# Kernel optimization log

Measured on AMD Instinct MI355X. Metric: run time of the kernel, lower is better.

Reference implementation:

```python
import jax, jax.numpy as jnp
import numpy as np

S, B, P, E = 2048, 128, 1024, 192  # seq len, batch, single_eval_pos, embedding_size
NAN_IND, INF_IND, NEG_INF_IND = -2.0, 2.0, 4.0


def setup_inputs() -> dict:
    key = jax.random.key(0)
    k1, k2, k3 = jax.random.split(key, 3)
    y = jax.random.normal(k1, (S, B, 1), jnp.float32)
    # nn.Linear(in_features=2, out_features=E): weight [E, 2], bias [E]
    W = jax.random.normal(k2, (E, 2), jnp.float32) * 0.1
    b = jax.random.normal(k3, (E,), jnp.float32) * 0.1
    return {"y": y, "W": W, "b": b, "single_eval_pos": P}


def reference(y, W, b, single_eval_pos):
    sep = single_eval_pos
    # --- nan handling (nan_handling_y_encoder=True) ---
    prefix = y[:sep]                              # [P, B, 1]
    means = jnp.nanmean(prefix, axis=0)           # [B, 1] (torch.nanmean ignores NaN only)
    is_nan = jnp.isnan(y)
    is_inf = jnp.isinf(y)
    mask = is_nan | is_inf
    indicators = (is_nan * NAN_IND
                  + (is_inf & (y > 0)) * INF_IND
                  + (is_inf & (y < 0)) * NEG_INF_IND).astype(y.dtype)  # [S, B, 1]
    y_imp = jnp.where(mask, means[None], y)       # [S, B, 1]

    # --- multiclass rank encode (max_num_classes >= 2) ---
    # torch: rank[t,b] = #{distinct values v in train prefix of column b : v < y[t,b]}
    col = y_imp[..., 0]                           # [S, B]
    s = jnp.sort(col[:sep], axis=0)               # [P, B] sorted train prefix per batch
    # marker of first occurrence of each distinct value in the sorted prefix
    is_new = jnp.concatenate(
        [jnp.ones((1, s.shape[1]), bool), s[1:] != s[:-1]], axis=0)  # [P, B]
    # [S, P, B] boolean compare, masked to distinct values, reduce over P
    cmp = (col[:, None, :] > s[None, :, :]) & is_new[None]
    ranks = cmp.sum(axis=1).astype(y.dtype)[..., None]  # [S, B, 1]

    x = jnp.concatenate([ranks, indicators], axis=-1)   # [S, B, 2]
    return x @ W.T + b                                   # [S, B, E]
```

## Files before the change

### kernel.cpp

```cpp
#include <hip/hip_runtime.h>
#include <math.h>

#define S_DIM 2048
#define B_DIM 128
#define P_DIM 1024
#define E_DIM 192
#define SB    (S_DIM * B_DIM)

typedef float f32x4 __attribute__((ext_vector_type(4)));
typedef float f32x2 __attribute__((ext_vector_type(2)));

__global__ __launch_bounds__(256) void prep_rank_kernel(
    const float* __restrict__ y, const int* __restrict__ sep_p,
    f32x2* __restrict__ ri) {
  __shared__ float sm[P_DIM];
  __shared__ float su[P_DIM];
  __shared__ float redf[256];
  __shared__ int   redi[256];
  __shared__ int   scan[256];
  __shared__ int   Ksh;

  const int b   = blockIdx.x;
  const int tid = threadIdx.x;
  const int sep = *sep_p;

  float lsum = 0.f;
  int   lcnt = 0;
  for (int i = tid; i < P_DIM; i += 256) {
    float v = (i < sep) ? y[i * B_DIM + b] : INFINITY;
    sm[i] = v;
    if (i < sep && !isnan(v)) { lsum += v; lcnt++; }
  }
  redf[tid] = lsum;
  redi[tid] = lcnt;
  __syncthreads();
  for (int off = 128; off > 0; off >>= 1) {
    if (tid < off) { redf[tid] += redf[tid + off]; redi[tid] += redi[tid + off]; }
    __syncthreads();
  }
  const float mean = redf[0] / (float)redi[0];

  for (int i = tid; i < sep; i += 256) {
    float v = sm[i];
    if (isnan(v) || isinf(v)) sm[i] = mean;
  }
  __syncthreads();

  for (int k = 2; k <= P_DIM; k <<= 1) {
    for (int j = k >> 1; j > 0; j >>= 1) {
      for (int i = tid; i < P_DIM; i += 256) {
        int ixj = i ^ j;
        if (ixj > i) {
          float a = sm[i], c = sm[ixj];
          bool up = ((i & k) == 0);
          if (up ? (a > c) : (a < c)) { sm[i] = c; sm[ixj] = a; }
        }
      }
      __syncthreads();
    }
  }

  int flags[4];
  int lu = 0;
  for (int q = 0; q < 4; q++) {
    int i = tid * 4 + q;
    bool nw = (i == 0) || (sm[i] != sm[i - 1]);
    flags[q] = nw ? 1 : 0;
    lu += flags[q];
  }
  scan[tid] = lu;
  __syncthreads();
  for (int off = 1; off < 256; off <<= 1) {
    int t = (tid >= off) ? scan[tid - off] : 0;
    __syncthreads();
    scan[tid] += t;
    __syncthreads();
  }
  int excl = scan[tid] - lu;
  for (int q = 0; q < 4; q++) {
    int i = tid * 4 + q;
    if (flags[q]) { su[excl] = sm[i]; excl++; }
  }
  if (tid == 255) Ksh = scan[255];
  __syncthreads();

  const int K = Ksh;

  for (int s = tid; s < S_DIM; s += 256) {
    const float v = y[s * B_DIM + b];
    float ind = 0.f;
    float x = v;
    if (isnan(v))      { ind = -2.f; x = mean; }
    else if (isinf(v)) { ind = (v > 0.f) ? 2.f : 4.f; x = mean; }
    int lo = 0, hi = K;
    while (lo < hi) {
      int mid = (lo + hi) >> 1;
      if (su[mid] < x) lo = mid + 1; else hi = mid;
    }
    f32x2 rv; rv.x = (float)lo; rv.y = ind;
    ri[b * S_DIM + s] = rv;
  }
}

__global__ __launch_bounds__(192) void out_kernel(
    const f32x2* __restrict__ ri, const f32x4* __restrict__ Wf,
    const f32x4* __restrict__ bias4, f32x4* __restrict__ out) {
  const int q  = threadIdx.x % 48;
  const int r0 = threadIdx.x / 48;
  const f32x4 wa = Wf[2 * q];
  const f32x4 wb = Wf[2 * q + 1];
  const f32x4 bb = bias4[q];
  const int stride = gridDim.x * 4;
  for (int sb = blockIdx.x * 4 + r0; sb < SB; sb += stride) {
    const int s = sb >> 7;
    const int b = sb & (B_DIM - 1);
    const f32x2 rv = ri[b * S_DIM + s];
    f32x4 o;
    o.x = fmaf(rv.x, wa.x, fmaf(rv.y, wa.y, bb.x));
    o.y = fmaf(rv.x, wa.z, fmaf(rv.y, wa.w, bb.y));
    o.z = fmaf(rv.x, wb.x, fmaf(rv.y, wb.y, bb.z));
    o.w = fmaf(rv.x, wb.z, fmaf(rv.y, wb.w, bb.w));
    __builtin_nontemporal_store(o, &out[(size_t)sb * 48 + q]);
  }
}

extern "C" void kernel_launch(void* const* d_in, const int* in_sizes, int n_in,
                              void* d_out, int out_size, void* d_ws, size_t ws_size,
                              hipStream_t stream) {
  const float* y    = (const float*)d_in[0];
  const float* W    = (const float*)d_in[1];
  const float* bias = (const float*)d_in[2];
  const int*   sep  = (const int*)d_in[3];

  f32x2* ri = (f32x2*)d_ws;

  prep_rank_kernel<<<B_DIM, 256, 0, stream>>>(y, sep, ri);

  out_kernel<<<4096, 192, 0, stream>>>(ri, (const f32x4*)W,
                                       (const f32x4*)bias, (f32x4*)d_out);
}
```

Baseline: 253.4 us.

## Restructure rank prep with 1024-thread register bitonic sort and warp primitives

The prep kernel now runs one element per thread with 1024 threads per block. The bitonic sort keeps values in registers, using wave shuffles for strides under 64 and shared memory only for larger strides. The mean reduction and the dedupe prefix scan now use wave shuffle, ballot and popcount in place of barrier-heavy shared-memory trees. The aim is to cut the many __syncthreads rounds and LDS traffic in the serial per-batch prep, at the cost of larger blocks and a fixed assumption that P equals the block size.

```diff
diff --git a/kernel.cpp b/kernel.cpp
--- a/kernel.cpp
+++ b/kernel.cpp
@@ -10,88 +10,86 @@
 typedef float f32x4 __attribute__((ext_vector_type(4)));
 typedef float f32x2 __attribute__((ext_vector_type(2)));
 
-__global__ __launch_bounds__(256) void prep_rank_kernel(
+__global__ __launch_bounds__(1024) void prep_rank_kernel(
     const float* __restrict__ y, const int* __restrict__ sep_p,
     f32x2* __restrict__ ri) {
   __shared__ float sm[P_DIM];
   __shared__ float su[P_DIM];
-  __shared__ float redf[256];
-  __shared__ int   redi[256];
-  __shared__ int   scan[256];
+  __shared__ float wred[16];
+  __shared__ int   wredi[16];
+  __shared__ int   wbase[16];
   __shared__ int   Ksh;
+  __shared__ float meansh;
 
-  const int b   = blockIdx.x;
-  const int tid = threadIdx.x;
-  const int sep = *sep_p;
+  const int tid  = threadIdx.x;
+  const int lane = tid & 63;
+  const int w    = tid >> 6;
+  const int b    = blockIdx.x;
+  const int sep  = *sep_p;
 
-  float lsum = 0.f;
-  int   lcnt = 0;
-  for (int i = tid; i < P_DIM; i += 256) {
-    float v = (i < sep) ? y[i * B_DIM + b] : INFINITY;
-    sm[i] = v;
-    if (i < sep && !isnan(v)) { lsum += v; lcnt++; }
+  float v = (tid < sep) ? y[tid * B_DIM + b] : INFINITY;
+  const bool valid = (tid < sep) && !isnan(v);
+  float sv = valid ? v : 0.f;
+  int   ci = valid ? 1 : 0;
+  for (int off = 32; off; off >>= 1) {
+    sv += __shfl_down(sv, off);
+    ci += __shfl_down(ci, off);
   }
-  redf[tid] = lsum;
-  redi[tid] = lcnt;
+  if (lane == 0) { wred[w] = sv; wredi[w] = ci; }
   __syncthreads();
-  for (int off = 128; off > 0; off >>= 1) {
-    if (tid < off) { redf[tid] += redf[tid + off]; redi[tid] += redi[tid + off]; }
-    __syncthreads();
-  }
-  const float mean = redf[0] / (float)redi[0];
-
-  for (int i = tid; i < sep; i += 256) {
-    float v = sm[i];
-    if (isnan(v) || isinf(v)) sm[i] = mean;
+  if (tid == 0) {
+    float s = 0.f; int c = 0;
+    for (int i = 0; i < 16; i++) { s += wred[i]; c += wredi[i]; }
+    meansh = s / (float)c;
   }
   __syncthreads();
+  const float mean = meansh;
+
+  if (tid < sep && (isnan(v) || isinf(v))) v = mean;
 
   for (int k = 2; k <= P_DIM; k <<= 1) {
-    for (int j = k >> 1; j > 0; j >>= 1) {
-      for (int i = tid; i < P_DIM; i += 256) {
-        int ixj = i ^ j;
-        if (ixj > i) {
-          float a = sm[i], c = sm[ixj];
-          bool up = ((i & k) == 0);
-          if (up ? (a > c) : (a < c)) { sm[i] = c; sm[ixj] = a; }
-        }
+    for (int j = k >> 1; j; j >>= 1) {
+      float pv;
+      if (j >= 64) {
+        sm[tid] = v;
+        __syncthreads();
+        pv = sm[tid ^ j];
+        __syncthreads();
+      } else {
+        pv = __shfl_xor(v, j);
       }
-      __syncthreads();
+      const bool up    = ((tid & k) == 0);
+      const bool lower = ((tid & j) == 0);
+      const float mn = fminf(v, pv), mx = fmaxf(v, pv);
+      v = (up == lower) ? mn : mx;
     }
   }
 
-  int flags[4];
-  int lu = 0;
-  for (int q = 0; q < 4; q++) {
-    int i = tid * 4 + q;
-    bool nw = (i == 0) || (sm[i] != sm[i - 1]);
-    flags[q] = nw ? 1 : 0;
-    lu += flags[q];
+  sm[tid] = v;
+  __syncthreads();
+  const bool flag = (tid == 0) || (v != sm[tid - 1]);
+  const unsigned long long mask = __ballot(flag);
+  const int lower = __popcll(mask & ((1ull << lane) - 1ull));
+  const int wcnt  = __popcll(mask);
+  if (lane == 0) wbase[w] = wcnt;
+  __syncthreads();
+  if (tid == 0) {
+    int acc = 0;
+    for (int i = 0; i < 16; i++) { int t = wbase[i]; wbase[i] = acc; acc += t; }
+    Ksh = acc;
   }
-  scan[tid] = lu;
   __syncthreads();
-  for (int off = 1; off < 256; off <<= 1) {
-    int t = (tid >= off) ? scan[tid - off] : 0;
-    __syncthreads();
-    scan[tid] += t;
-    __syncthreads();
-  }
-  int excl = scan[tid] - lu;
-  for (int q = 0; q < 4; q++) {
-    int i = tid * 4 + q;
-    if (flags[q]) { su[excl] = sm[i]; excl++; }
-  }
-  if (tid == 255) Ksh = scan[255];
+  if (flag) su[wbase[w] + lower] = v;
   __syncthreads();
-
   const int K = Ksh;
 
-  for (int s = tid; s < S_DIM; s += 256) {
-    const float v = y[s * B_DIM + b];
+  for (int it = 0; it < 2; ++it) {
+    const int s = it * P_DIM + tid;
+    const float q = y[s * B_DIM + b];
     float ind = 0.f;
-    float x = v;
-    if (isnan(v))      { ind = -2.f; x = mean; }
-    else if (isinf(v)) { ind = (v > 0.f) ? 2.f : 4.f; x = mean; }
+    float x = q;
+    if (isnan(q))      { ind = -2.f; x = mean; }
+    else if (isinf(q)) { ind = (q > 0.f) ? 2.f : 4.f; x = mean; }
     int lo = 0, hi = K;
     while (lo < hi) {
       int mid = (lo + hi) >> 1;
@@ -134,7 +132,7 @@
 
   f32x2* ri = (f32x2*)d_ws;
 
-  prep_rank_kernel<<<B_DIM, 256, 0, stream>>>(y, sep, ri);
+  prep_rank_kernel<<<B_DIM, 1024, 0, stream>>>(y, sep, ri);
 
   out_kernel<<<4096, 192, 0, stream>>>(ri, (const f32x4*)W,
                                        (const f32x4*)bias, (f32x4*)d_out);
```

Result: faster. 222.1 us (-12.4%).
